# Performance work log

Measured on AMD Instinct MI355X. Metric: run time of the kernel, lower is better.

Reference implementation:

```python
import jax, jax.numpy as jnp
import numpy as np
import math

B, S, D, H, HD, M, E = 4, 1024, 1024, 16, 64, 4096, 1024
EPS = 1e-6

def rms_norm(x, w):
    # torch: x / (||x||/sqrt(d) + eps) * w  (eps added to the norm, not norm^2)
    n = jnp.sqrt(jnp.sum(x * x, axis=-1, keepdims=True)) / math.sqrt(x.shape[-1])
    return x / (n + EPS) * w

def rope(x):
    # x: (B,H,S,hd)
    hd, s = x.shape[-1], x.shape[2]
    inv = 1.0 / (10000.0 ** (jnp.arange(0, hd, 2, dtype=jnp.float32) / hd))
    fr = jnp.arange(s, dtype=jnp.float32)[:, None] * inv[None, :]        # (S, hd/2)
    emb = jnp.concatenate([fr, fr], axis=-1)                              # (S, hd)
    cos, sin = jnp.cos(emb), jnp.sin(emb)
    x1, x2 = x[..., : hd // 2], x[..., hd // 2 :]
    rot = jnp.concatenate([-x2, x1], axis=-1)
    return x * cos + rot * sin

def setup_inputs() -> dict:
    key = jax.random.key(0)
    ks = jax.random.split(key, 18)
    p = lambda k, sh: jax.random.normal(k, sh, jnp.float32) * 0.02
    return {
        'x': jax.random.normal(ks[0], (B, S, D), jnp.float32),
        'emb': jax.random.normal(ks[1], (B, E), jnp.float32),
        'ln1_w': jnp.ones((D,), jnp.float32),
        'ln1_lW': p(ks[2], (E, 2 * D)), 'ln1_lb': p(ks[3], (2 * D,)),
        'ln2_w': jnp.ones((D,), jnp.float32),
        'ln2_lW': p(ks[4], (E, 2 * D)), 'ln2_lb': p(ks[5], (2 * D,)),
        'qkv_W': p(ks[6], (D, 3 * D)), 'qkv_b': p(ks[7], (3 * D,)),
        'proj_W': p(ks[8], (D, D)), 'proj_b': p(ks[9], (D,)),
        'nq_w': jnp.ones((HD,), jnp.float32), 'nk_w': jnp.ones((HD,), jnp.float32),
        'mlp_W': p(ks[10], (D, 2 * M)), 'mlp_b': p(ks[11], (2 * M,)),
        'out_W': p(ks[12], (M, D)), 'out_b': p(ks[13], (D,)),
        'gates_W': p(ks[14], (E, 2 * D)), 'gates_b': p(ks[15], (2 * D,)),
    }

def reference(x, emb, ln1_w, ln1_lW, ln1_lb, ln2_w, ln2_lW, ln2_lb,
              qkv_W, qkv_b, proj_W, proj_b, nq_w, nk_w,
              mlp_W, mlp_b, out_W, out_b, gates_W, gates_b):
    g = emb @ gates_W + gates_b                       # (B, 2D)
    gate_mha, gate_mlp = g[:, :D], g[:, D:]
    # AdaLNZero 1
    ss = emb @ ln1_lW + ln1_lb                        # (B, 2D): [scale | shift]
    xn = rms_norm(x, ln1_w) * (1.0 + ss[:, None, :D]) + ss[:, None, D:]
    # RoPE attention with qk RMSNorm
    qkv = (xn @ qkv_W + qkv_b).reshape(B, S, 3, H, HD).transpose(2, 0, 3, 1, 4)
    q, k, v = qkv[0], qkv[1], qkv[2]                  # each (B,H,S,HD)
    q = rms_norm(rope(q), nq_w)
    k = rms_norm(rope(k), nk_w)
    scores = jnp.einsum('bhqd,bhkd->bhqk', q, k) * (HD ** -0.5)
    attn = jnp.nan_to_num(jax.nn.softmax(scores, axis=-1))
    ao = jnp.einsum('bhqk,bhkd->bhqd', attn, v).transpose(0, 2, 1, 3).reshape(B, S, D)
    x = x + gate_mha[:, None, :] * (ao @ proj_W + proj_b)
    # AdaLNZero 2 + SwiGLU MLP
    ss2 = emb @ ln2_lW + ln2_lb
    xn2 = rms_norm(x, ln2_w) * (1.0 + ss2[:, None, :D]) + ss2[:, None, D:]
    h = xn2 @ mlp_W + mlp_b                           # (B,S,2M)
    act = h[..., :M] * jax.nn.silu(h[..., M:])
    mlp_out = act @ out_W + out_b
    return x + gate_mlp[:, None, :] * mlp_out
```

## Files before the change

### kernel.cpp

```cpp
#include <hip/hip_runtime.h>
#include <hip/hip_bf16.h>
#include <math.h>

#define B_ 4
#define S_ 1024
#define D_ 1024
#define H_ 16
#define HD_ 64
#define M_ 4096
#define E_ 1024

using bf16 = __hip_bfloat16;
typedef short bf16x8 __attribute__((ext_vector_type(8)));
typedef float f32x4 __attribute__((ext_vector_type(4)));

__device__ __forceinline__ void gl_lds16(const void* g, void* l) {
    __builtin_amdgcn_global_load_lds(
        (__attribute__((address_space(1))) void*)(g),
        (__attribute__((address_space(3))) void*)(l), 16, 0, 0);
}


__global__ __launch_bounds__(256) void transpose_kernel(
    const float* __restrict__ W, bf16* __restrict__ Wt, int K, int N)
{
    __shared__ float tile[32][33];
    int n0 = blockIdx.x * 32, k0 = blockIdx.y * 32;
    int tx = threadIdx.x & 31, ty = threadIdx.x >> 5;
    #pragma unroll
    for (int r = ty; r < 32; r += 8)
        tile[r][tx] = W[(long)(k0 + r) * N + n0 + tx];
    __syncthreads();
    #pragma unroll
    for (int r = ty; r < 32; r += 8)
        Wt[(long)(n0 + r) * K + k0 + tx] = __float2bfloat16(tile[tx][r]);
}

__global__ __launch_bounds__(256) void embgemm_kernel(
    const float* __restrict__ emb,
    const float* __restrict__ W0, const float* __restrict__ b0,
    const float* __restrict__ W1, const float* __restrict__ b1,
    const float* __restrict__ W2, const float* __restrict__ b2,
    float* __restrict__ G, float* __restrict__ SS, float* __restrict__ SS2)
{
    __shared__ float se[1024];
    int b = blockIdx.y;
    for (int i = threadIdx.x; i < 1024; i += 256) se[i] = emb[b * 1024 + i];
    __syncthreads();
    int j = blockIdx.x * 256 + threadIdx.x;
    int which = j >> 11, col = j & 2047;
    const float* W  = which == 0 ? W0 : (which == 1 ? W1 : W2);
    const float* bb = which == 0 ? b0 : (which == 1 ? b1 : b2);
    float acc = bb[col];
    for (int k = 0; k < 1024; ++k) acc += se[k] * W[(long)k * 2048 + col];
    float* out = which == 0 ? G : (which == 1 ? SS : SS2);
    out[b * 2048 + col] = acc;
}

__global__ __launch_bounds__(256) void rmsmod_kernel(
    const float* __restrict__ x, const float* __restrict__ w,
    const float* __restrict__ ss, bf16* __restrict__ out)
{
    int row = blockIdx.x;
    int b = row >> 10;
    const float* xr = x + (long)row * D_;
    float4 v = ((const float4*)xr)[threadIdx.x];
    float ssum = v.x * v.x + v.y * v.y + v.z * v.z + v.w * v.w;
    #pragma unroll
    for (int off = 32; off; off >>= 1) ssum += __shfl_xor(ssum, off);
    __shared__ float red[4];
    if ((threadIdx.x & 63) == 0) red[threadIdx.x >> 6] = ssum;
    __syncthreads();
    float tot = red[0] + red[1] + red[2] + red[3];
    float n = sqrtf(tot) * (1.f / 32.f);
    float inv = 1.f / (n + 1e-6f);
    int d0 = threadIdx.x * 4;
    const float* ssb = ss + b * 2048;
    bf16 t[4];
    t[0] = __float2bfloat16(v.x * inv * w[d0 + 0] * (1.f + ssb[d0 + 0]) + ssb[D_ + d0 + 0]);
    t[1] = __float2bfloat16(v.y * inv * w[d0 + 1] * (1.f + ssb[d0 + 1]) + ssb[D_ + d0 + 1]);
    t[2] = __float2bfloat16(v.z * inv * w[d0 + 2] * (1.f + ssb[d0 + 2]) + ssb[D_ + d0 + 2]);
    t[3] = __float2bfloat16(v.w * inv * w[d0 + 3] * (1.f + ssb[d0 + 3]) + ssb[D_ + d0 + 3]);
    *(uint2*)&out[(long)row * D_ + d0] = *(uint2*)t;
}

__global__ __launch_bounds__(256) void gemm_kernel(
    const bf16* __restrict__ A, const bf16* __restrict__ Bt,
    const float* __restrict__ bias,
    bf16* __restrict__ Cb, float* __restrict__ Cf,
    const float* __restrict__ resid, const float* __restrict__ gates, int gate_off,
    int Mrows, int N, int K, int mode)
{
    __shared__ bf16 sA[128 * 32];
    __shared__ bf16 sB[128 * 32];
    const int tid = threadIdx.x;
    const int wave = tid >> 6, lane = tid & 63;
    const int num_pid_n = N >> 7;
    const int pid = blockIdx.x;
    const int group_size = 8 * num_pid_n;
    const int group_id = pid / group_size;
    const int pid_in = pid - group_id * group_size;
    const int pid_m = group_id * 8 + (pid_in & 7);
    const int pid_n = pid_in >> 3;
    const int m0 = pid_m * 128, n0 = pid_n * 128;
    const int wm = (wave & 1) * 64, wn = (wave >> 1) * 64;
    const int cl = lane & 15, qd = lane >> 4;

    f32x4 acc[4][4] = {};

    const int c0 = wave * 128 + lane, c1 = c0 + 64;
    const int r0 = c0 >> 2, s0 = (c0 & 3) ^ ((c0 >> 3) & 3);
    const int r1 = c1 >> 2, s1 = (c1 & 3) ^ ((c1 >> 3) & 3);
    const bf16* gA0 = A + (long)(m0 + r0) * K + s0 * 8;
    const bf16* gA1 = A + (long)(m0 + r1) * K + s1 * 8;
    const bf16* gB0 = Bt + (long)(n0 + r0) * K + s0 * 8;
    const bf16* gB1 = Bt + (long)(n0 + r1) * K + s1 * 8;
    bf16* lA0 = &sA[wave * 1024];
    bf16* lA1 = &sA[wave * 1024 + 512];
    bf16* lB0 = &sB[wave * 1024];
    bf16* lB1 = &sB[wave * 1024 + 512];

    const int q8s = (qd ^ ((cl >> 1) & 3)) * 8;

    for (int kc = 0; kc < K; kc += 32) {
        gl_lds16(gA0 + kc, lA0);
        gl_lds16(gA1 + kc, lA1);
        gl_lds16(gB0 + kc, lB0);
        gl_lds16(gB1 + kc, lB1);
        __syncthreads();
        bf16x8 af[4], bfr[4];
        #pragma unroll
        for (int t = 0; t < 4; ++t)
            af[t] = *(const bf16x8*)&sA[(wm + cl + t * 16) * 32 + q8s];
        #pragma unroll
        for (int u = 0; u < 4; ++u)
            bfr[u] = *(const bf16x8*)&sB[(wn + cl + u * 16) * 32 + q8s];
        #pragma unroll
        for (int t = 0; t < 4; ++t)
            #pragma unroll
            for (int u = 0; u < 4; ++u)
                acc[t][u] = __builtin_amdgcn_mfma_f32_16x16x32_bf16(af[t], bfr[u], acc[t][u], 0, 0, 0);
        __syncthreads();
    }

    #pragma unroll
    for (int t = 0; t < 4; ++t) {
        #pragma unroll
        for (int u = 0; u < 4; ++u) {
            int col = n0 + wn + u * 16 + cl;
            float bs = bias[col];
            #pragma unroll
            for (int i = 0; i < 4; ++i) {
                int row = m0 + wm + t * 16 + qd * 4 + i;
                float v = acc[t][u][i] + bs;
                if (mode == 0) {
                    Cb[(long)row * N + col] = __float2bfloat16(v);
                } else {
                    int b = row >> 10;
                    float g = gates[b * 2048 + gate_off + col];
                    Cf[(long)row * N + col] = resid[(long)row * N + col] + g * v;
                }
            }
        }
    }
}

__global__ __launch_bounds__(256) void gemm_mlp_kernel(
    const bf16* __restrict__ A, const bf16* __restrict__ Bt,
    const float* __restrict__ bias, bf16* __restrict__ ACT)
{
    __shared__ bf16 sA[128 * 32];
    __shared__ bf16 sB1[64 * 32];
    __shared__ bf16 sB2[64 * 32];
    const int tid = threadIdx.x;
    const int wave = tid >> 6, lane = tid & 63;
    const int num_pid_n = 64;
    const int pid = blockIdx.x;
    const int group_size = 8 * num_pid_n;
    const int group_id = pid / group_size;
    const int pid_in = pid - group_id * group_size;
    const int pid_m = group_id * 8 + (pid_in & 7);
    const int pid_n = pid_in >> 3;
    const int m0 = pid_m * 128, n0 = pid_n * 64;
    const int wm = (wave & 1) * 64, wn = (wave >> 1) * 32;
    const int cl = lane & 15, qd = lane >> 4;
    const int K = 1024;

    f32x4 acc1[4][2] = {};
    f32x4 acc2[4][2] = {};

    const int c0 = wave * 128 + lane, c1 = c0 + 64;
    const int ra0 = c0 >> 2, sa0 = (c0 & 3) ^ ((c0 >> 3) & 3);
    const int ra1 = c1 >> 2, sa1 = (c1 & 3) ^ ((c1 >> 3) & 3);
    const int rb = tid >> 2, sb = (tid & 3) ^ ((tid >> 3) & 3);
    const bf16* gA0 = A + (long)(m0 + ra0) * K + sa0 * 8;
    const bf16* gA1 = A + (long)(m0 + ra1) * K + sa1 * 8;
    const bf16* gB1 = Bt + (long)(n0 + rb) * K + sb * 8;
    const bf16* gB2 = Bt + (long)(4096 + n0 + rb) * K + sb * 8;
    bf16* lA0 = &sA[wave * 1024];
    bf16* lA1 = &sA[wave * 1024 + 512];
    bf16* lB1 = &sB1[wave * 512];
    bf16* lB2 = &sB2[wave * 512];

    const int q8s = (qd ^ ((cl >> 1) & 3)) * 8;

    for (int kc = 0; kc < K; kc += 32) {
        gl_lds16(gA0 + kc, lA0);
        gl_lds16(gA1 + kc, lA1);
        gl_lds16(gB1 + kc, lB1);
        gl_lds16(gB2 + kc, lB2);
        __syncthreads();
        bf16x8 af[4], b1[2], b2[2];
        #pragma unroll
        for (int t = 0; t < 4; ++t)
            af[t] = *(const bf16x8*)&sA[(wm + cl + t * 16) * 32 + q8s];
        #pragma unroll
        for (int u = 0; u < 2; ++u) {
            b1[u] = *(const bf16x8*)&sB1[(wn + cl + u * 16) * 32 + q8s];
            b2[u] = *(const bf16x8*)&sB2[(wn + cl + u * 16) * 32 + q8s];
        }
        #pragma unroll
        for (int t = 0; t < 4; ++t)
            #pragma unroll
            for (int u = 0; u < 2; ++u) {
                acc1[t][u] = __builtin_amdgcn_mfma_f32_16x16x32_bf16(af[t], b1[u], acc1[t][u], 0, 0, 0);
                acc2[t][u] = __builtin_amdgcn_mfma_f32_16x16x32_bf16(af[t], b2[u], acc2[t][u], 0, 0, 0);
            }
        __syncthreads();
    }

    #pragma unroll
    for (int t = 0; t < 4; ++t) {
        #pragma unroll
        for (int u = 0; u < 2; ++u) {
            int col = n0 + wn + u * 16 + cl;
            float bs1 = bias[col];
            float bs2 = bias[4096 + col];
            #pragma unroll
            for (int i = 0; i < 4; ++i) {
                int row = m0 + wm + t * 16 + qd * 4 + i;
                float h1 = acc1[t][u][i] + bs1;
                float h2 = acc2[t][u][i] + bs2;
                float sg = 1.f / (1.f + __expf(-h2));
                ACT[(long)row * 4096 + col] = __float2bfloat16(h1 * h2 * sg);
            }
        }
    }
}

__global__ __launch_bounds__(256) void gemm64_kernel(
    const bf16* __restrict__ A, const bf16* __restrict__ Bt,
    const float* __restrict__ bias,
    bf16* __restrict__ Cb, float* __restrict__ Cf,
    const float* __restrict__ resid, const float* __restrict__ gates, int gate_off,
    int Mrows, int N, int K, int mode)
{
    __shared__ bf16 sA[64 * 32];
    __shared__ bf16 sB[64 * 32];
    const int tid = threadIdx.x;
    const int wave = tid >> 6, lane = tid & 63;
    const int num_pid_n = N >> 6;
    const int pid = blockIdx.x;
    const int group_size = 8 * num_pid_n;
    const int group_id = pid / group_size;
    const int pid_in = pid - group_id * group_size;
    const int pid_m = group_id * 8 + (pid_in & 7);
    const int pid_n = pid_in >> 3;
    const int m0 = pid_m * 64, n0 = pid_n * 64;
    const int wm = (wave & 1) * 32, wn = (wave >> 1) * 32;
    const int cl = lane & 15, qd = lane >> 4;

    f32x4 acc[2][2] = {};

    const int c = tid;
    const int rr = c >> 2, ss = (c & 3) ^ ((c >> 3) & 3);
    const bf16* gA = A + (long)(m0 + rr) * K + ss * 8;
    const bf16* gB = Bt + (long)(n0 + rr) * K + ss * 8;
    bf16* lA = &sA[wave * 512];
    bf16* lB = &sB[wave * 512];

    const int q8s = (qd ^ ((cl >> 1) & 3)) * 8;

    for (int kc = 0; kc < K; kc += 32) {
        gl_lds16(gA + kc, lA);
        gl_lds16(gB + kc, lB);
        __syncthreads();
        bf16x8 af[2], bfr[2];
        #pragma unroll
        for (int t = 0; t < 2; ++t)
            af[t] = *(const bf16x8*)&sA[(wm + cl + t * 16) * 32 + q8s];
        #pragma unroll
        for (int u = 0; u < 2; ++u)
            bfr[u] = *(const bf16x8*)&sB[(wn + cl + u * 16) * 32 + q8s];
        #pragma unroll
        for (int t = 0; t < 2; ++t)
            #pragma unroll
            for (int u = 0; u < 2; ++u)
                acc[t][u] = __builtin_amdgcn_mfma_f32_16x16x32_bf16(af[t], bfr[u], acc[t][u], 0, 0, 0);
        __syncthreads();
    }

    #pragma unroll
    for (int t = 0; t < 2; ++t) {
        #pragma unroll
        for (int u = 0; u < 2; ++u) {
            int col = n0 + wn + u * 16 + cl;
            float bs = bias[col];
            #pragma unroll
            for (int i = 0; i < 4; ++i) {
                int row = m0 + wm + t * 16 + qd * 4 + i;
                float v = acc[t][u][i] + bs;
                if (mode == 0) {
                    Cb[(long)row * N + col] = __float2bfloat16(v);
                } else {
                    int b = row >> 10;
                    float g = gates[b * 2048 + gate_off + col];
                    Cf[(long)row * N + col] = resid[(long)row * N + col] + g * v;
                }
            }
        }
    }
}

__global__ __launch_bounds__(256) void ropenorm_kernel(
    const bf16* __restrict__ qkv, const float* __restrict__ nq_w, const float* __restrict__ nk_w,
    bf16* __restrict__ qh, bf16* __restrict__ kh, bf16* __restrict__ vt)
{
    int gid = blockIdx.x * 4 + (threadIdx.x >> 6);
    int lane = threadIdx.x & 63;
    int b = gid >> 14, s = (gid >> 4) & (S_ - 1), h = gid & (H_ - 1);
    const long base = (long)(b * S_ + s) * 3072 + h * 64 + lane;
    float qv = __bfloat162float(qkv[base]);
    float kv = __bfloat162float(qkv[base + 1024]);
    float vv = __bfloat162float(qkv[base + 2048]);
    int j = lane & 31;
    float inv = exp2f(-(float)j * (13.287712379549449f / 32.f));
    float ang = (float)s * inv;
    float sn, c;
    sincosf(ang, &sn, &c);
    float pq = __shfl_xor(qv, 32);
    float pk = __shfl_xor(kv, 32);
    float rq = (lane < 32) ? -pq : pq;
    float rk = (lane < 32) ? -pk : pk;
    float qr = qv * c + rq * sn;
    float kr = kv * c + rk * sn;
    float sq = qr * qr, sk = kr * kr;
    #pragma unroll
    for (int off = 32; off; off >>= 1) { sq += __shfl_xor(sq, off); sk += __shfl_xor(sk, off); }
    float nq = sqrtf(sq) * 0.125f;
    float nk = sqrtf(sk) * 0.125f;
    float qo = qr / (nq + 1e-6f) * nq_w[lane];
    float ko = kr / (nk + 1e-6f) * nk_w[lane];
    long hb = ((long)(b * H_ + h) * S_ + s) * 64 + lane;
    qh[hb] = __float2bfloat16(qo);
    kh[hb] = __float2bfloat16(ko);
    vt[((long)(b * H_ + h) * 64 + lane) * S_ + s] = __float2bfloat16(vv);
}

__global__ __launch_bounds__(256) void attn_kernel(
    const bf16* __restrict__ qh, const bf16* __restrict__ kh, const bf16* __restrict__ vt,
    bf16* __restrict__ ao)
{
    const int bh = blockIdx.y;
    const int q0 = blockIdx.x * 64;
    const int tid = threadIdx.x, wave = tid >> 6, lane = tid & 63;
    const int cl = lane & 15, qd = lane >> 4;

    __shared__ bf16 sQ[64 * 72];
    __shared__ bf16 sK[64 * 72];
    __shared__ bf16 sV[64 * 72];
    __shared__ bf16 sP[4][16 * 72];

    {
        const bf16* Qg = qh + (long)bh * S_ * 64 + (long)q0 * 64;
        int a = tid, b2 = tid + 256;
        *(uint4*)&sQ[(a >> 3) * 72 + (a & 7) * 8]  = *(const uint4*)&Qg[(a >> 3) * 64 + (a & 7) * 8];
        *(uint4*)&sQ[(b2 >> 3) * 72 + (b2 & 7) * 8] = *(const uint4*)&Qg[(b2 >> 3) * 64 + (b2 & 7) * 8];
    }

    float m_i[4], l_i[4];
    f32x4 o_acc[4] = {};
    #pragma unroll
    for (int i = 0; i < 4; ++i) { m_i[i] = -1e30f; l_i[i] = 0.f; }

    const bf16* Kg = kh + (long)bh * S_ * 64;
    const bf16* Vg = vt + (long)bh * 64 * S_;

    for (int kv0 = 0; kv0 < S_; kv0 += 64) {
        __syncthreads();
        {
            int a = tid, b2 = tid + 256;
            *(uint4*)&sK[(a >> 3) * 72 + (a & 7) * 8]   = *(const uint4*)&Kg[((long)kv0 + (a >> 3)) * 64 + (a & 7) * 8];
            *(uint4*)&sK[(b2 >> 3) * 72 + (b2 & 7) * 8] = *(const uint4*)&Kg[((long)kv0 + (b2 >> 3)) * 64 + (b2 & 7) * 8];
            *(uint4*)&sV[(a >> 3) * 72 + (a & 7) * 8]   = *(const uint4*)&Vg[(long)(a >> 3) * S_ + kv0 + (a & 7) * 8];
            *(uint4*)&sV[(b2 >> 3) * 72 + (b2 & 7) * 8] = *(const uint4*)&Vg[(long)(b2 >> 3) * S_ + kv0 + (b2 & 7) * 8];
        }
        __syncthreads();

        f32x4 sfr[4] = {};
        #pragma unroll
        for (int u = 0; u < 4; ++u) {
            #pragma unroll
            for (int ks = 0; ks < 2; ++ks) {
                bf16x8 aq = *(const bf16x8*)&sQ[(wave * 16 + cl) * 72 + ks * 32 + qd * 8];
                bf16x8 bk = *(const bf16x8*)&sK[(u * 16 + cl) * 72 + ks * 32 + qd * 8];
                sfr[u] = __builtin_amdgcn_mfma_f32_16x16x32_bf16(aq, bk, sfr[u], 0, 0, 0);
            }
        }

        float mnew[4], al[4];
        #pragma unroll
        for (int i = 0; i < 4; ++i) {
            float mx = m_i[i];
            #pragma unroll
            for (int u = 0; u < 4; ++u) {
                float s0 = sfr[u][i] * 0.125f;
                sfr[u][i] = s0;
                mx = fmaxf(mx, s0);
            }
            mx = fmaxf(mx, __shfl_xor(mx, 1));
            mx = fmaxf(mx, __shfl_xor(mx, 2));
            mx = fmaxf(mx, __shfl_xor(mx, 4));
            mx = fmaxf(mx, __shfl_xor(mx, 8));
            mnew[i] = mx;
            al[i] = __expf(m_i[i] - mx);
            m_i[i] = mx;
        }
        #pragma unroll
        for (int i = 0; i < 4; ++i) {
            float sum = 0.f;
            #pragma unroll
            for (int u = 0; u < 4; ++u) {
                float p = __expf(sfr[u][i] - mnew[i]);
                sum += p;
                sP[wave][(qd * 4 + i) * 72 + u * 16 + cl] = __float2bfloat16(p);
            }
            sum += __shfl_xor(sum, 1);
            sum += __shfl_xor(sum, 2);
            sum += __shfl_xor(sum, 4);
            sum += __shfl_xor(sum, 8);
            l_i[i] = l_i[i] * al[i] + sum;
        }
        #pragma unroll
        for (int u = 0; u < 4; ++u)
            #pragma unroll
            for (int i = 0; i < 4; ++i) o_acc[u][i] *= al[i];

        #pragma unroll
        for (int ks = 0; ks < 2; ++ks) {
            bf16x8 ap = *(const bf16x8*)&sP[wave][cl * 72 + ks * 32 + qd * 8];
            #pragma unroll
            for (int u = 0; u < 4; ++u) {
                bf16x8 bv = *(const bf16x8*)&sV[(u * 16 + cl) * 72 + ks * 32 + qd * 8];
                o_acc[u] = __builtin_amdgcn_mfma_f32_16x16x32_bf16(ap, bv, o_acc[u], 0, 0, 0);
            }
        }
    }

    #pragma unroll
    for (int i = 0; i < 4; ++i) {
        float invl = 1.f / l_i[i];
        int row = q0 + wave * 16 + qd * 4 + i;
        #pragma unroll
        for (int u = 0; u < 4; ++u) {
            int d = u * 16 + cl;
            ao[((long)(bh >> 4) * S_ + row) * D_ + (bh & 15) * 64 + d] =
                __float2bfloat16(o_acc[u][i] * invl);
        }
    }
}

extern "C" void kernel_launch(void* const* d_in, const int* in_sizes, int n_in,
                              void* d_out, int out_size, void* d_ws, size_t ws_size,
                              hipStream_t stream) {
    const float* x       = (const float*)d_in[0];
    const float* emb     = (const float*)d_in[1];
    const float* ln1_w   = (const float*)d_in[2];
    const float* ln1_lW  = (const float*)d_in[3];
    const float* ln1_lb  = (const float*)d_in[4];
    const float* ln2_w   = (const float*)d_in[5];
    const float* ln2_lW  = (const float*)d_in[6];
    const float* ln2_lb  = (const float*)d_in[7];
    const float* qkv_W   = (const float*)d_in[8];
    const float* qkv_b   = (const float*)d_in[9];
    const float* proj_W  = (const float*)d_in[10];
    const float* proj_b  = (const float*)d_in[11];
    const float* nq_w    = (const float*)d_in[12];
    const float* nk_w    = (const float*)d_in[13];
    const float* mlp_W   = (const float*)d_in[14];
    const float* mlp_b   = (const float*)d_in[15];
    const float* out_W   = (const float*)d_in[16];
    const float* out_b   = (const float*)d_in[17];
    const float* gates_W = (const float*)d_in[18];
    const float* gates_b = (const float*)d_in[19];
    float* out = (float*)d_out;

    char* p = (char*)d_ws;
    if (ws_size < 159481856UL) return;
    bf16* WT_QKV  = (bf16*)p;  p += 6291456;
    bf16* WT_PROJ = (bf16*)p;  p += 2097152;
    bf16* WT_MLP  = (bf16*)p;  p += 16777216;
    bf16* WT_OUT  = (bf16*)p;  p += 8388608;
    float* G      = (float*)p; p += 32768;
    float* SSb    = (float*)p; p += 32768;
    float* SS2b   = (float*)p; p += 32768;
    float* X1     = (float*)p; p += 16777216;
    bf16* XN2     = (bf16*)p;  p += 8388608;
    bf16* ACT     = (bf16*)p;  p += 33554432;
    char* REG = p;
    bf16* XN   = (bf16*)(REG);
    bf16* QKV  = (bf16*)(REG + 8388608);
    bf16* QH   = (bf16*)(REG + 33554432);
    bf16* KH   = (bf16*)(REG + 41943040);
    bf16* VT   = (bf16*)(REG + 50331648);
    bf16* AO   = (bf16*)(REG + 58720256);

    dim3 blk(256);
    transpose_kernel<<<dim3(96, 32),  blk, 0, stream>>>(qkv_W,  WT_QKV, 1024, 3072);
    transpose_kernel<<<dim3(32, 32),  blk, 0, stream>>>(proj_W, WT_PROJ, 1024, 1024);
    transpose_kernel<<<dim3(256, 32), blk, 0, stream>>>(mlp_W,  WT_MLP, 1024, 8192);
    transpose_kernel<<<dim3(32, 128), blk, 0, stream>>>(out_W,  WT_OUT, 4096, 1024);
    embgemm_kernel<<<dim3(24, 4), blk, 0, stream>>>(emb, gates_W, gates_b, ln1_lW, ln1_lb,
                                                    ln2_lW, ln2_lb, G, SSb, SS2b);
    rmsmod_kernel<<<dim3(4096), blk, 0, stream>>>(x, ln1_w, SSb, XN);
    gemm_kernel<<<dim3(768), blk, 0, stream>>>(XN, WT_QKV, qkv_b, QKV, nullptr,
                                               nullptr, nullptr, 0, 4096, 3072, 1024, 0);
    ropenorm_kernel<<<dim3(16384), blk, 0, stream>>>(QKV, nq_w, nk_w, QH, KH, VT);
    attn_kernel<<<dim3(16, 64), blk, 0, stream>>>(QH, KH, VT, AO);
    gemm64_kernel<<<dim3(1024), blk, 0, stream>>>(AO, WT_PROJ, proj_b, nullptr, X1,
                                                  x, G, 0, 4096, 1024, 1024, 1);
    rmsmod_kernel<<<dim3(4096), blk, 0, stream>>>(X1, ln2_w, SS2b, XN2);
    gemm_mlp_kernel<<<dim3(2048), blk, 0, stream>>>(XN2, WT_MLP, mlp_b, ACT);
    gemm64_kernel<<<dim3(1024), blk, 0, stream>>>(ACT, WT_OUT, out_b, nullptr, out,
                                                  X1, G, 1024, 4096, 1024, 4096, 1);
}
```

Baseline: 536.9 us.

## Split-K the embedding GEMM with atomics and widen proj/out GEMM tiles

```diff
diff --git a/kernel.cpp b/kernel.cpp
--- a/kernel.cpp
+++ b/kernel.cpp
@@ -43,18 +43,20 @@
     const float* __restrict__ W2, const float* __restrict__ b2,
     float* __restrict__ G, float* __restrict__ SS, float* __restrict__ SS2)
 {
-    __shared__ float se[1024];
+    __shared__ float se[256];
     int b = blockIdx.y;
-    for (int i = threadIdx.x; i < 1024; i += 256) se[i] = emb[b * 1024 + i];
+    int k0 = blockIdx.z * 256;
+    if (threadIdx.x < 256) se[threadIdx.x] = emb[b * 1024 + k0 + threadIdx.x];
     __syncthreads();
     int j = blockIdx.x * 256 + threadIdx.x;
     int which = j >> 11, col = j & 2047;
     const float* W  = which == 0 ? W0 : (which == 1 ? W1 : W2);
     const float* bb = which == 0 ? b0 : (which == 1 ? b1 : b2);
-    float acc = bb[col];
-    for (int k = 0; k < 1024; ++k) acc += se[k] * W[(long)k * 2048 + col];
+    float acc = (k0 == 0) ? bb[col] : 0.f;
+    #pragma unroll 4
+    for (int k = 0; k < 256; ++k) acc += se[k] * W[(long)(k0 + k) * 2048 + col];
     float* out = which == 0 ? G : (which == 1 ? SS : SS2);
-    out[b * 2048 + col] = acc;
+    atomicAdd(&out[b * 2048 + col], acc);
 }
 
 __global__ __launch_bounds__(256) void rmsmod_kernel(
@@ -248,14 +250,14 @@
     }
 }
 
-__global__ __launch_bounds__(256) void gemm64_kernel(
+__global__ __launch_bounds__(256) void gemm_wide_kernel(
     const bf16* __restrict__ A, const bf16* __restrict__ Bt,
     const float* __restrict__ bias,
     bf16* __restrict__ Cb, float* __restrict__ Cf,
     const float* __restrict__ resid, const float* __restrict__ gates, int gate_off,
     int Mrows, int N, int K, int mode)
 {
-    __shared__ bf16 sA[64 * 32];
+    __shared__ bf16 sA[128 * 32];
     __shared__ bf16 sB[64 * 32];
     const int tid = threadIdx.x;
     const int wave = tid >> 6, lane = tid & 63;
@@ -266,34 +268,39 @@
     const int pid_in = pid - group_id * group_size;
     const int pid_m = group_id * 8 + (pid_in & 7);
     const int pid_n = pid_in >> 3;
-    const int m0 = pid_m * 64, n0 = pid_n * 64;
-    const int wm = (wave & 1) * 32, wn = (wave >> 1) * 32;
+    const int m0 = pid_m * 128, n0 = pid_n * 64;
+    const int wm = (wave & 1) * 64, wn = (wave >> 1) * 32;
     const int cl = lane & 15, qd = lane >> 4;
 
-    f32x4 acc[2][2] = {};
-
-    const int c = tid;
-    const int rr = c >> 2, ss = (c & 3) ^ ((c >> 3) & 3);
-    const bf16* gA = A + (long)(m0 + rr) * K + ss * 8;
-    const bf16* gB = Bt + (long)(n0 + rr) * K + ss * 8;
-    bf16* lA = &sA[wave * 512];
+    f32x4 acc[4][2] = {};
+
+    const int c0 = wave * 128 + lane, c1 = c0 + 64;
+    const int ra0 = c0 >> 2, sa0 = (c0 & 3) ^ ((c0 >> 3) & 3);
+    const int ra1 = c1 >> 2, sa1 = (c1 & 3) ^ ((c1 >> 3) & 3);
+    const int rb = tid >> 2, sb = (tid & 3) ^ ((tid >> 3) & 3);
+    const bf16* gA0 = A + (long)(m0 + ra0) * K + sa0 * 8;
+    const bf16* gA1 = A + (long)(m0 + ra1) * K + sa1 * 8;
+    const bf16* gB = Bt + (long)(n0 + rb) * K + sb * 8;
+    bf16* lA0 = &sA[wave * 1024];
+    bf16* lA1 = &sA[wave * 1024 + 512];
     bf16* lB = &sB[wave * 512];
 
     const int q8s = (qd ^ ((cl >> 1) & 3)) * 8;
 
     for (int kc = 0; kc < K; kc += 32) {
-        gl_lds16(gA + kc, lA);
+        gl_lds16(gA0 + kc, lA0);
+        gl_lds16(gA1 + kc, lA1);
         gl_lds16(gB + kc, lB);
         __syncthreads();
-        bf16x8 af[2], bfr[2];
-        #pragma unroll
-        for (int t = 0; t < 2; ++t)
+        bf16x8 af[4], bfr[2];
+        #pragma unroll
+        for (int t = 0; t < 4; ++t)
             af[t] = *(const bf16x8*)&sA[(wm + cl + t * 16) * 32 + q8s];
         #pragma unroll
         for (int u = 0; u < 2; ++u)
             bfr[u] = *(const bf16x8*)&sB[(wn + cl + u * 16) * 32 + q8s];
         #pragma unroll
-        for (int t = 0; t < 2; ++t)
+        for (int t = 0; t < 4; ++t)
             #pragma unroll
             for (int u = 0; u < 2; ++u)
                 acc[t][u] = __builtin_amdgcn_mfma_f32_16x16x32_bf16(af[t], bfr[u], acc[t][u], 0, 0, 0);
@@ -301,7 +308,7 @@
     }
 
     #pragma unroll
-    for (int t = 0; t < 2; ++t) {
+    for (int t = 0; t < 4; ++t) {
         #pragma unroll
         for (int u = 0; u < 2; ++u) {
             int col = n0 + wn + u * 16 + cl;
@@ -516,21 +523,22 @@
     bf16* AO   = (bf16*)(REG + 58720256);
 
     dim3 blk(256);
+    hipMemsetAsync(G, 0, 98304, stream);
     transpose_kernel<<<dim3(96, 32),  blk, 0, stream>>>(qkv_W,  WT_QKV, 1024, 3072);
     transpose_kernel<<<dim3(32, 32),  blk, 0, stream>>>(proj_W, WT_PROJ, 1024, 1024);
     transpose_kernel<<<dim3(256, 32), blk, 0, stream>>>(mlp_W,  WT_MLP, 1024, 8192);
     transpose_kernel<<<dim3(32, 128), blk, 0, stream>>>(out_W,  WT_OUT, 4096, 1024);
-    embgemm_kernel<<<dim3(24, 4), blk, 0, stream>>>(emb, gates_W, gates_b, ln1_lW, ln1_lb,
-                                                    ln2_lW, ln2_lb, G, SSb, SS2b);
+    embgemm_kernel<<<dim3(24, 4, 4), blk, 0, stream>>>(emb, gates_W, gates_b, ln1_lW, ln1_lb,
+                                                       ln2_lW, ln2_lb, G, SSb, SS2b);
     rmsmod_kernel<<<dim3(4096), blk, 0, stream>>>(x, ln1_w, SSb, XN);
     gemm_kernel<<<dim3(768), blk, 0, stream>>>(XN, WT_QKV, qkv_b, QKV, nullptr,
                                                nullptr, nullptr, 0, 4096, 3072, 1024, 0);
     ropenorm_kernel<<<dim3(16384), blk, 0, stream>>>(QKV, nq_w, nk_w, QH, KH, VT);
     attn_kernel<<<dim3(16, 64), blk, 0, stream>>>(QH, KH, VT, AO);
-    gemm64_kernel<<<dim3(1024), blk, 0, stream>>>(AO, WT_PROJ, proj_b, nullptr, X1,
-                                                  x, G, 0, 4096, 1024, 1024, 1);
+    gemm_wide_kernel<<<dim3(512), blk, 0, stream>>>(AO, WT_PROJ, proj_b, nullptr, X1,
+                                                    x, G, 0, 4096, 1024, 1024, 1);
     rmsmod_kernel<<<dim3(4096), blk, 0, stream>>>(X1, ln2_w, SS2b, XN2);
     gemm_mlp_kernel<<<dim3(2048), blk, 0, stream>>>(XN2, WT_MLP, mlp_b, ACT);
-    gemm64_kernel<<<dim3(1024), blk, 0, stream>>>(ACT, WT_OUT, out_b, nullptr, out,
-                                                  X1, G, 1024, 4096, 1024, 4096, 1);
-}
+    gemm_wide_kernel<<<dim3(512), blk, 0, stream>>>(ACT, WT_OUT, out_b, nullptr, out,
+                                                    X1, G, 1024, 4096, 1024, 4096, 1);
+}
```

Result: slower. 556.5 us (+3.7%).

## Split-K the output GEMM and embedding GEMM with atomic accumulation

Applied to the files above, without the earlier changes.

```diff
diff --git a/kernel.cpp b/kernel.cpp
--- a/kernel.cpp
+++ b/kernel.cpp
@@ -43,18 +43,20 @@
     const float* __restrict__ W2, const float* __restrict__ b2,
     float* __restrict__ G, float* __restrict__ SS, float* __restrict__ SS2)
 {
-    __shared__ float se[1024];
+    __shared__ float se[256];
     int b = blockIdx.y;
-    for (int i = threadIdx.x; i < 1024; i += 256) se[i] = emb[b * 1024 + i];
+    int k0 = blockIdx.z * 256;
+    if (threadIdx.x < 256) se[threadIdx.x] = emb[b * 1024 + k0 + threadIdx.x];
     __syncthreads();
     int j = blockIdx.x * 256 + threadIdx.x;
     int which = j >> 11, col = j & 2047;
     const float* W  = which == 0 ? W0 : (which == 1 ? W1 : W2);
     const float* bb = which == 0 ? b0 : (which == 1 ? b1 : b2);
-    float acc = bb[col];
-    for (int k = 0; k < 1024; ++k) acc += se[k] * W[(long)k * 2048 + col];
+    float acc = (k0 == 0) ? bb[col] : 0.f;
+    #pragma unroll 4
+    for (int k = 0; k < 256; ++k) acc += se[k] * W[(long)(k0 + k) * 2048 + col];
     float* out = which == 0 ? G : (which == 1 ? SS : SS2);
-    out[b * 2048 + col] = acc;
+    atomicAdd(&out[b * 2048 + col], acc);
 }
 
 __global__ __launch_bounds__(256) void rmsmod_kernel(
@@ -147,6 +149,158 @@
     for (int t = 0; t < 4; ++t) {
         #pragma unroll
         for (int u = 0; u < 4; ++u) {
+            int col = n0 + wn + u * 16 + cl;
+            float bs = bias[col];
+            #pragma unroll
+            for (int i = 0; i < 4; ++i) {
+                int row = m0 + wm + t * 16 + qd * 4 + i;
+                float v = acc[t][u][i] + bs;
+                if (mode == 0) {
+                    Cb[(long)row * N + col] = __float2bfloat16(v);
+                } else {
+                    int b = row >> 10;
+                    float g = gates[b * 2048 + gate_off + col];
+                    Cf[(long)row * N + col] = resid[(long)row * N + col] + g * v;
+                }
+            }
+        }
+    }
+}
+
+__global__ __launch_bounds__(256) void gemm_splitk_kernel(
+    const bf16* __restrict__ A, const bf16* __restrict__ Bt,
+    const float* __restrict__ bias,
+    float* __restrict__ Cf,
+    const float* __restrict__ resid, const float* __restrict__ gates, int gate_off,
+    int N, int Ktot, int KS, int zbits)
+{
+    __shared__ bf16 sA[128 * 32];
+    __shared__ bf16 sB[128 * 32];
+    const int tid = threadIdx.x;
+    const int wave = tid >> 6, lane = tid & 63;
+    const int pid = blockIdx.x;
+    const int z = pid & ((1 << zbits) - 1);
+    const int tile = pid >> zbits;
+    const int num_pid_n = N >> 7;
+    const int pid_m = tile / num_pid_n;
+    const int pid_n = tile - pid_m * num_pid_n;
+    const int m0 = pid_m * 128, n0 = pid_n * 128;
+    const int wm = (wave & 1) * 64, wn = (wave >> 1) * 64;
+    const int cl = lane & 15, qd = lane >> 4;
+    const long kbeg = (long)z * KS;
+
+    f32x4 acc[4][4] = {};
+
+    const int c0 = wave * 128 + lane, c1 = c0 + 64;
+    const int r0 = c0 >> 2, s0 = (c0 & 3) ^ ((c0 >> 3) & 3);
+    const int r1 = c1 >> 2, s1 = (c1 & 3) ^ ((c1 >> 3) & 3);
+    const bf16* gA0 = A + (long)(m0 + r0) * Ktot + kbeg + s0 * 8;
+    const bf16* gA1 = A + (long)(m0 + r1) * Ktot + kbeg + s1 * 8;
+    const bf16* gB0 = Bt + (long)(n0 + r0) * Ktot + kbeg + s0 * 8;
+    const bf16* gB1 = Bt + (long)(n0 + r1) * Ktot + kbeg + s1 * 8;
+    bf16* lA0 = &sA[wave * 1024];
+    bf16* lA1 = &sA[wave * 1024 + 512];
+    bf16* lB0 = &sB[wave * 1024];
+    bf16* lB1 = &sB[wave * 1024 + 512];
+
+    const int q8s = (qd ^ ((cl >> 1) & 3)) * 8;
+
+    for (int kc = 0; kc < KS; kc += 32) {
+        gl_lds16(gA0 + kc, lA0);
+        gl_lds16(gA1 + kc, lA1);
+        gl_lds16(gB0 + kc, lB0);
+        gl_lds16(gB1 + kc, lB1);
+        __syncthreads();
+        bf16x8 af[4], bfr[4];
+        #pragma unroll
+        for (int t = 0; t < 4; ++t)
+            af[t] = *(const bf16x8*)&sA[(wm + cl + t * 16) * 32 + q8s];
+        #pragma unroll
+        for (int u = 0; u < 4; ++u)
+            bfr[u] = *(const bf16x8*)&sB[(wn + cl + u * 16) * 32 + q8s];
+        #pragma unroll
+        for (int t = 0; t < 4; ++t)
+            #pragma unroll
+            for (int u = 0; u < 4; ++u)
+                acc[t][u] = __builtin_amdgcn_mfma_f32_16x16x32_bf16(af[t], bfr[u], acc[t][u], 0, 0, 0);
+        __syncthreads();
+    }
+
+    #pragma unroll
+    for (int t = 0; t < 4; ++t) {
+        #pragma unroll
+        for (int u = 0; u < 4; ++u) {
+            int col = n0 + wn + u * 16 + cl;
+            float bs = bias[col];
+            #pragma unroll
+            for (int i = 0; i < 4; ++i) {
+                int row = m0 + wm + t * 16 + qd * 4 + i;
+                int b = row >> 10;
+                float g = gates[b * 2048 + gate_off + col];
+                float add = g * acc[t][u][i];
+                if (z == 0) add += resid[(long)row * N + col] + g * bs;
+                atomicAdd(&Cf[(long)row * N + col], add);
+            }
+        }
+    }
+}
+
+__global__ __launch_bounds__(256) void gemm64_kernel(
+    const bf16* __restrict__ A, const bf16* __restrict__ Bt,
+    const float* __restrict__ bias,
+    bf16* __restrict__ Cb, float* __restrict__ Cf,
+    const float* __restrict__ resid, const float* __restrict__ gates, int gate_off,
+    int Mrows, int N, int K, int mode)
+{
+    __shared__ bf16 sA[64 * 32];
+    __shared__ bf16 sB[64 * 32];
+    const int tid = threadIdx.x;
+    const int wave = tid >> 6, lane = tid & 63;
+    const int num_pid_n = N >> 6;
+    const int pid = blockIdx.x;
+    const int group_size = 8 * num_pid_n;
+    const int group_id = pid / group_size;
+    const int pid_in = pid - group_id * group_size;
+    const int pid_m = group_id * 8 + (pid_in & 7);
+    const int pid_n = pid_in >> 3;
+    const int m0 = pid_m * 64, n0 = pid_n * 64;
+    const int wm = (wave & 1) * 32, wn = (wave >> 1) * 32;
+    const int cl = lane & 15, qd = lane >> 4;
+
+    f32x4 acc[2][2] = {};
+
+    const int c = tid;
+    const int rr = c >> 2, ss = (c & 3) ^ ((c >> 3) & 3);
+    const bf16* gA = A + (long)(m0 + rr) * K + ss * 8;
+    const bf16* gB = Bt + (long)(n0 + rr) * K + ss * 8;
+    bf16* lA = &sA[wave * 512];
+    bf16* lB = &sB[wave * 512];
+
+    const int q8s = (qd ^ ((cl >> 1) & 3)) * 8;
+
+    for (int kc = 0; kc < K; kc += 32) {
+        gl_lds16(gA + kc, lA);
+        gl_lds16(gB + kc, lB);
+        __syncthreads();
+        bf16x8 af[2], bfr[2];
+        #pragma unroll
+        for (int t = 0; t < 2; ++t)
+            af[t] = *(const bf16x8*)&sA[(wm + cl + t * 16) * 32 + q8s];
+        #pragma unroll
+        for (int u = 0; u < 2; ++u)
+            bfr[u] = *(const bf16x8*)&sB[(wn + cl + u * 16) * 32 + q8s];
+        #pragma unroll
+        for (int t = 0; t < 2; ++t)
+            #pragma unroll
+            for (int u = 0; u < 2; ++u)
+                acc[t][u] = __builtin_amdgcn_mfma_f32_16x16x32_bf16(af[t], bfr[u], acc[t][u], 0, 0, 0);
+        __syncthreads();
+    }
+
+    #pragma unroll
+    for (int t = 0; t < 2; ++t) {
+        #pragma unroll
+        for (int u = 0; u < 2; ++u) {
             int col = n0 + wn + u * 16 + cl;
             float bs = bias[col];
             #pragma unroll
@@ -243,80 +397,6 @@
                 float h2 = acc2[t][u][i] + bs2;
                 float sg = 1.f / (1.f + __expf(-h2));
                 ACT[(long)row * 4096 + col] = __float2bfloat16(h1 * h2 * sg);
-            }
-        }
-    }
-}
-
-__global__ __launch_bounds__(256) void gemm64_kernel(
-    const bf16* __restrict__ A, const bf16* __restrict__ Bt,
-    const float* __restrict__ bias,
-    bf16* __restrict__ Cb, float* __restrict__ Cf,
-    const float* __restrict__ resid, const float* __restrict__ gates, int gate_off,
-    int Mrows, int N, int K, int mode)
-{
-    __shared__ bf16 sA[64 * 32];
-    __shared__ bf16 sB[64 * 32];
-    const int tid = threadIdx.x;
-    const int wave = tid >> 6, lane = tid & 63;
-    const int num_pid_n = N >> 6;
-    const int pid = blockIdx.x;
-    const int group_size = 8 * num_pid_n;
-    const int group_id = pid / group_size;
-    const int pid_in = pid - group_id * group_size;
-    const int pid_m = group_id * 8 + (pid_in & 7);
-    const int pid_n = pid_in >> 3;
-    const int m0 = pid_m * 64, n0 = pid_n * 64;
-    const int wm = (wave & 1) * 32, wn = (wave >> 1) * 32;
-    const int cl = lane & 15, qd = lane >> 4;
-
-    f32x4 acc[2][2] = {};
-
-    const int c = tid;
-    const int rr = c >> 2, ss = (c & 3) ^ ((c >> 3) & 3);
-    const bf16* gA = A + (long)(m0 + rr) * K + ss * 8;
-    const bf16* gB = Bt + (long)(n0 + rr) * K + ss * 8;
-    bf16* lA = &sA[wave * 512];
-    bf16* lB = &sB[wave * 512];
-
-    const int q8s = (qd ^ ((cl >> 1) & 3)) * 8;
-
-    for (int kc = 0; kc < K; kc += 32) {
-        gl_lds16(gA + kc, lA);
-        gl_lds16(gB + kc, lB);
-        __syncthreads();
-        bf16x8 af[2], bfr[2];
-        #pragma unroll
-        for (int t = 0; t < 2; ++t)
-            af[t] = *(const bf16x8*)&sA[(wm + cl + t * 16) * 32 + q8s];
-        #pragma unroll
-        for (int u = 0; u < 2; ++u)
-            bfr[u] = *(const bf16x8*)&sB[(wn + cl + u * 16) * 32 + q8s];
-        #pragma unroll
-        for (int t = 0; t < 2; ++t)
-            #pragma unroll
-            for (int u = 0; u < 2; ++u)
-                acc[t][u] = __builtin_amdgcn_mfma_f32_16x16x32_bf16(af[t], bfr[u], acc[t][u], 0, 0, 0);
-        __syncthreads();
-    }
-
-    #pragma unroll
-    for (int t = 0; t < 2; ++t) {
-        #pragma unroll
-        for (int u = 0; u < 2; ++u) {
-            int col = n0 + wn + u * 16 + cl;
-            float bs = bias[col];
-            #pragma unroll
-            for (int i = 0; i < 4; ++i) {
-                int row = m0 + wm + t * 16 + qd * 4 + i;
-                float v = acc[t][u][i] + bs;
-                if (mode == 0) {
-                    Cb[(long)row * N + col] = __float2bfloat16(v);
-                } else {
-                    int b = row >> 10;
-                    float g = gates[b * 2048 + gate_off + col];
-                    Cf[(long)row * N + col] = resid[(long)row * N + col] + g * v;
-                }
             }
         }
     }
@@ -516,12 +596,14 @@
     bf16* AO   = (bf16*)(REG + 58720256);
 
     dim3 blk(256);
+    hipMemsetAsync(G, 0, 98304, stream);
+    hipMemsetAsync(out, 0, (size_t)out_size * 4, stream);
     transpose_kernel<<<dim3(96, 32),  blk, 0, stream>>>(qkv_W,  WT_QKV, 1024, 3072);
     transpose_kernel<<<dim3(32, 32),  blk, 0, stream>>>(proj_W, WT_PROJ, 1024, 1024);
     transpose_kernel<<<dim3(256, 32), blk, 0, stream>>>(mlp_W,  WT_MLP, 1024, 8192);
     transpose_kernel<<<dim3(32, 128), blk, 0, stream>>>(out_W,  WT_OUT, 4096, 1024);
-    embgemm_kernel<<<dim3(24, 4), blk, 0, stream>>>(emb, gates_W, gates_b, ln1_lW, ln1_lb,
-                                                    ln2_lW, ln2_lb, G, SSb, SS2b);
+    embgemm_kernel<<<dim3(24, 4, 4), blk, 0, stream>>>(emb, gates_W, gates_b, ln1_lW, ln1_lb,
+                                                       ln2_lW, ln2_lb, G, SSb, SS2b);
     rmsmod_kernel<<<dim3(4096), blk, 0, stream>>>(x, ln1_w, SSb, XN);
     gemm_kernel<<<dim3(768), blk, 0, stream>>>(XN, WT_QKV, qkv_b, QKV, nullptr,
                                                nullptr, nullptr, 0, 4096, 3072, 1024, 0);
@@ -531,6 +613,6 @@
                                                   x, G, 0, 4096, 1024, 1024, 1);
     rmsmod_kernel<<<dim3(4096), blk, 0, stream>>>(X1, ln2_w, SS2b, XN2);
     gemm_mlp_kernel<<<dim3(2048), blk, 0, stream>>>(XN2, WT_MLP, mlp_b, ACT);
-    gemm64_kernel<<<dim3(1024), blk, 0, stream>>>(ACT, WT_OUT, out_b, nullptr, out,
-                                                  X1, G, 1024, 4096, 1024, 4096, 1);
-}
+    gemm_splitk_kernel<<<dim3(1024), blk, 0, stream>>>(ACT, WT_OUT, out_b, out,
+                                                       X1, G, 1024, 1024, 4096, 1024, 2);
+}
```

Result: slower. 582.7 us (+8.5%).
